# Optimization experiments

Measured on AMD Instinct MI355X. Metric: run time of the kernel, lower is better.

## Reference

```python
import jax, jax.numpy as jnp
import numpy as np

IDIM = 128   # idim == odim (fc1 input dim must match shift-slice width idim_q)
HDIM = 1024
CDIM = 256
IGNORE_OUT = 10000.0


def setup_inputs() -> dict:
    key = jax.random.key(0)
    ks = jax.random.split(key, 4)
    B, T = 4, 512
    x = jax.random.normal(ks[0], (B, T, IDIM), dtype=jnp.float32)
    y = jax.random.normal(ks[1], (B, T, IDIM), dtype=jnp.float32)
    # xavier-ish init for the two linears (bias zeroed, as in initialize())
    w1 = jax.random.normal(ks[2], (HDIM, IDIM), dtype=jnp.float32) / np.sqrt(IDIM).astype(np.float32)
    b1 = jnp.zeros((HDIM,), jnp.float32)
    w2 = jax.random.normal(ks[3], (IDIM, HDIM), dtype=jnp.float32) / np.sqrt(HDIM).astype(np.float32)
    b2 = jnpts = jnp.zeros((IDIM,), jnp.float32)
    return {"x": x, "y": y, "w1": w1, "b1": b1, "w2": w2, "b2": b2}


def _shift_stack(key_seq, idim):
    """Vectorized _pad_for_shift: (B,T,idim) -> (B,T,2*idim-1,idim) shifted slices."""
    pad = idim - 1
    kp = jnp.pad(key_seq, ((0, 0), (0, 0), (pad, pad)))  # (B,T,3*idim-2)
    idx = jnp.arange(2 * idim - 1)[:, None] + jnp.arange(idim)[None, :]  # (S, idim)
    return kp[..., idx]  # (B,T,S,idim)


def _forward(x, y, w1, b1, w2, b2):
    idim = IDIM
    n_iter = HDIM // CDIM
    seq_mask = (y == IGNORE_OUT)                      # (B,T,odim)
    denom = jnp.sum(~seq_mask).astype(x.dtype)
    y_res, x_res = y, x
    losses = []
    for i in range(n_iter):
        # --- argaug (scale=False): sliding cosine cross-correlation + argmax ---
        kpt = _shift_stack(x_res, idim)               # (B,T,S,idim), S=2*idim-1
        num = jnp.einsum('btd,btsd->bts', y_res, kpt)
        den = jnp.linalg.norm(y_res, axis=-1)[..., None] * jnp.linalg.norm(kpt, axis=-1)
        sim = jnp.where(den == 0, 0.0, num / jnp.where(den == 0, 1.0, den))  # NaN(0/0) -> 0
        idx = jnp.argmax(sim, axis=-1)                # (B,T), first max like torch.max
        x_aug = jnp.take_along_axis(kpt, idx[..., None, None], axis=2)[..., 0, :]  # (B,T,idim)
        # --- attention (detached) ---
        attn = jax.lax.stop_gradient(jax.nn.softmax(x_aug * y_res, axis=-1))
        x_attn = x_aug * attn
        # --- _reverse_pad_for_shift: un-shift x_attn by 2*idim-2 - idx ---
        pad = idim - 1
        xap = jnp.pad(x_attn, ((0, 0), (0, 0), (pad, pad)))
        ridx = (2 * idim - 2 - idx)[..., None] + jnp.arange(idim)  # (B,T,idim)
        x_ele = jnp.take_along_axis(xap, ridx, axis=-1)
        # --- channel-masked two-layer MLP ---
        h = x_attn @ w1.T + b1                        # (B,T,hdim)
        m = jnp.zeros((HDIM,), x.dtype).at[i * CDIM:(i + 1) * CDIM].set(1.0)
        y_ele = (h * m) @ w2.T + b2                   # (B,T,odim)
        # --- masked MSE (sum of masked squared errors / #unmasked) ---
        sq = jnp.where(seq_mask, 0.0, (y_ele - y_res) ** 2)
        losses.append(jnp.sum(sq) / denom)
        y_res = y_res - y_ele
        x_res = x_res - x_ele
    return jnp.mean(jnp.stack(losses))


def reference(x, y, w1, b1, w2, b2):
    return _forward(x, y, w1, b1, w2, b2)
```

## Files before the change

### kernel.cpp

```cpp
#include <hip/hip_runtime.h>
#include <math.h>

#define NROWS   2048
#define NITER   4
#define IGNORE_OUT 10000.0f

__global__ __launch_bounds__(128)
void prepK(const float* __restrict__ w1, const float* __restrict__ b1,
           const float* __restrict__ w2, const float* __restrict__ b2,
           float* __restrict__ Mt2, float* __restrict__ biasT, float* __restrict__ acc){
  const int blk = blockIdx.x;
  const int u = threadIdx.x;
  if (blk < 512){
    int i = blk >> 7, o = blk & 127;
    const float* w1p = w1 + (i * 256) * 128 + u;
    const float* w2p = w2 + o * 1024 + i * 256;
    float a = 0.f;
    #pragma unroll 16
    for (int c = 0; c < 256; ++c) a = fmaf(w1p[c * 128], w2p[c], a);
    Mt2[(i * 128 + o) * 128 + u] = a;
  } else if (blk < 516){
    int i = blk - 512;
    const float* w2p = w2 + u * 1024 + i * 256;
    const float* b1p = b1 + i * 256;
    float a = b2[u];
    #pragma unroll 8
    for (int c = 0; c < 256; ++c) a = fmaf(b1p[c], w2p[c], a);
    biasT[i * 128 + u] = a;
  } else {
    if (u < 2) acc[u] = 0.f;
  }
}

__global__ __launch_bounds__(64, 2)
void mainK(const float* __restrict__ x, const float* __restrict__ y,
           const float* __restrict__ Mt2, const float* __restrict__ biasT,
           float* __restrict__ acc){
  __shared__ alignas(16) float xr[128];
  __shared__ alignas(16) float xatt[128];
  __shared__ float yd[384];

  const int l = threadIdx.x;
  const long base = (long)blockIdx.x * 128;

  float xv0 = x[base + l],      xv1 = x[base + 64 + l];
  float yv0 = y[base + l],      yv1 = y[base + 64 + l];
  const bool m0 = (yv0 == IGNORE_OUT), m1 = (yv1 == IGNORE_OUT);
  float cnt = (m0 ? 0.f : 1.f) + (m1 ? 0.f : 1.f);
  float lossAcc = 0.f;

  xr[l] = xv0; xr[64 + l] = xv1;
  yd[128 + l] = yv0; yd[192 + l] = yv1;
  yd[256 + l] = yv0; yd[320 + l] = yv1;
  __syncthreads();

  for (int i = 0; i < NITER; ++i){
    float s0 = xv0 * xv0, s1 = xv1 * xv1;
    #pragma unroll
    for (int o2 = 1; o2 < 64; o2 <<= 1){
      float t0 = __shfl_up(s0, o2, 64);
      float t1 = __shfl_up(s1, o2, 64);
      if (l >= o2){ s0 += t0; s1 += t1; }
    }
    float tot0  = __shfl(s0, 63, 64);
    float prefA = s0;
    float prefB = s1 + tot0;
    float total = __shfl(s1, 63, 64) + tot0;

    float ny = yv0 * yv0 + yv1 * yv1;
    #pragma unroll
    for (int o2 = 32; o2; o2 >>= 1) ny += __shfl_xor(ny, o2, 64);
    float nY = sqrtf(ny);

    const float* ydpA = yd + (255 - l);
    const float* ydpB = yd + (191 - l);
    float ntA = 0.f, n1A = 0.f, ntB = 0.f, n1B = 0.f;
    #pragma unroll 4
    for (int j4 = 0; j4 < 64; j4 += 4){
      float4 x4 = *(const float4*)&xr[j4];
      float xx[4] = {x4.x, x4.y, x4.z, x4.w};
      #pragma unroll
      for (int e = 0; e < 4; ++e){
        int j = j4 + e;
        float pA = ydpA[j] * xx[e];
        float pB = ydpB[j] * xx[e];
        ntA += pA; n1A += (j <= l) ? pA : 0.f;
        ntB += pB; n1B += pB;
      }
    }
    #pragma unroll 4
    for (int j4 = 64; j4 < 128; j4 += 4){
      float4 x4 = *(const float4*)&xr[j4];
      float xx[4] = {x4.x, x4.y, x4.z, x4.w};
      #pragma unroll
      for (int e = 0; e < 4; ++e){
        int j = j4 + e;
        float pA = ydpA[j] * xx[e];
        float pB = ydpB[j] * xx[e];
        ntA += pA;
        ntB += pB; n1B += (j - 64 <= l) ? pB : 0.f;
      }
    }

    float bv; int bi;
    {
      float numA1 = n1A, numA2 = ntA - n1A;
      float numB1 = n1B, numB2 = ntB - n1B;
      float dA1 = nY * sqrtf(prefA);
      float dB1 = nY * sqrtf(prefB);
      float dA2 = nY * sqrtf(fmaxf(total - prefA, 0.f));
      float dB2 = nY * sqrtf(fmaxf(total - prefB, 0.f));
      float sA1 = (dA1 == 0.f) ? 0.f : numA1 / dA1;
      float sB1 = (dB1 == 0.f) ? 0.f : numB1 / dB1;
      float sA2 = (dA2 == 0.f) ? 0.f : numA2 / dA2;
      float sB2 = (dB2 == 0.f) ? 0.f : numB2 / dB2;
      if (l == 63) sB2 = -INFINITY;
      bv = sA1; bi = l;
      if (sB1 > bv){ bv = sB1; bi = l + 64;  }
      if (sA2 > bv){ bv = sA2; bi = l + 128; }
      if (sB2 > bv){ bv = sB2; bi = l + 192; }
    }
    #pragma unroll
    for (int o2 = 1; o2 < 64; o2 <<= 1){
      float ov = __shfl_xor(bv, o2, 64);
      int   oi = __shfl_xor(bi, o2, 64);
      if (ov > bv || (ov == bv && oi < bi)){ bv = ov; bi = oi; }
    }
    const int sstar = bi;

    int j0 = sstar + l - 127, j1 = j0 + 64;
    float xa0 = ((unsigned)j0 < 128u) ? xr[j0] : 0.f;
    float xa1 = ((unsigned)j1 < 128u) ? xr[j1] : 0.f;
    float z0 = xa0 * yv0, z1 = xa1 * yv1;
    float mz = fmaxf(z0, z1);
    #pragma unroll
    for (int o2 = 32; o2; o2 >>= 1) mz = fmaxf(mz, __shfl_xor(mz, o2, 64));
    float e0 = expf(z0 - mz), e1 = expf(z1 - mz);
    float se = e0 + e1;
    #pragma unroll
    for (int o2 = 32; o2; o2 >>= 1) se += __shfl_xor(se, o2, 64);
    float w0 = xa0 * (e0 / se), w1v = xa1 * (e1 / se);
    xatt[l] = w0; xatt[64 + l] = w1v;
    __syncthreads();

    int k0 = l + 127 - sstar, k1 = k0 + 64;
    xv0 -= ((unsigned)k0 < 128u) ? xatt[k0] : 0.f;
    xv1 -= ((unsigned)k1 < 128u) ? xatt[k1] : 0.f;
    xr[l] = xv0; xr[64 + l] = xv1;

    const float* MiA = Mt2 + (i * 128 + l) * 128;
    const float* MiB = MiA + 64 * 128;
    float aA = 0.f, aB = 0.f;
    #pragma unroll 4
    for (int d4 = 0; d4 < 128; d4 += 4){
      float4 xa4 = *(const float4*)&xatt[d4];
      float4 A4  = *(const float4*)&MiA[d4];
      float4 B4  = *(const float4*)&MiB[d4];
      aA = fmaf(A4.x, xa4.x, aA); aA = fmaf(A4.y, xa4.y, aA);
      aA = fmaf(A4.z, xa4.z, aA); aA = fmaf(A4.w, xa4.w, aA);
      aB = fmaf(B4.x, xa4.x, aB); aB = fmaf(B4.y, xa4.y, aB);
      aB = fmaf(B4.z, xa4.z, aB); aB = fmaf(B4.w, xa4.w, aB);
    }
    float ye0 = aA + biasT[i * 128 + l];
    float ye1 = aB + biasT[i * 128 + 64 + l];
    float d0 = ye0 - yv0, d1 = ye1 - yv1;
    if (!m0) lossAcc = fmaf(d0, d0, lossAcc);
    if (!m1) lossAcc = fmaf(d1, d1, lossAcc);
    yv0 = -d0; yv1 = -d1;
    yd[128 + l] = yv0; yd[192 + l] = yv1;
    yd[256 + l] = yv0; yd[320 + l] = yv1;
    __syncthreads();
  }

  #pragma unroll
  for (int o2 = 32; o2; o2 >>= 1){
    lossAcc += __shfl_xor(lossAcc, o2, 64);
    cnt     += __shfl_xor(cnt,     o2, 64);
  }
  if (l == 0){
    atomicAdd(&acc[0], lossAcc);
    atomicAdd(&acc[1], cnt);
  }
}

__global__ void finalize(const float* __restrict__ acc, float* __restrict__ out){
  if (threadIdx.x == 0 && blockIdx.x == 0)
    out[0] = acc[0] / ((float)NITER * acc[1]);
}

extern "C" void kernel_launch(void* const* d_in, const int* in_sizes, int n_in,
                              void* d_out, int out_size, void* d_ws, size_t ws_size,
                              hipStream_t stream){
  const float* x  = (const float*)d_in[0];
  const float* y  = (const float*)d_in[1];
  const float* w1 = (const float*)d_in[2];
  const float* b1 = (const float*)d_in[3];
  const float* w2 = (const float*)d_in[4];
  const float* b2 = (const float*)d_in[5];
  float* out = (float*)d_out;

  float* accp  = (float*)d_ws;
  float* Mt2   = (float*)((char*)d_ws + 256);
  float* biasT = (float*)((char*)d_ws + 256 + 4 * 128 * 128 * sizeof(float));

  prepK<<<517, 128, 0, stream>>>(w1, b1, w2, b2, Mt2, biasT, accp);
  mainK<<<NROWS, 64, 0, stream>>>(x, y, Mt2, biasT, accp);
  finalize<<<1, 64, 0, stream>>>(accp, out);
}
```

Baseline: 178.9 us.

## Process two rows per wave with register shuffles and fuse finalize via ticket

```diff
diff --git a/kernel.cpp b/kernel.cpp
--- a/kernel.cpp
+++ b/kernel.cpp
@@ -1,175 +1,246 @@
 #include <hip/hip_runtime.h>
 #include <math.h>
 
-#define NROWS   2048
-#define NITER   4
+#define NROWS 2048
+#define NBLK  1024
+#define NITER 4
 #define IGNORE_OUT 10000.0f
 
-__global__ __launch_bounds__(128)
+__device__ __forceinline__ float readlanef(float v, int lane){
+  return __int_as_float(__builtin_amdgcn_readlane(__float_as_int(v), lane));
+}
+__device__ __forceinline__ float rotup1(float v){
+  int i = __float_as_int(v);
+  return __int_as_float(__builtin_amdgcn_update_dpp(i, i, 0x13C, 0xF, 0xF, false));
+}
+__device__ __forceinline__ float gather128(float v0, float v1, int idx){
+  float g0 = __shfl(v0, idx & 63, 64);
+  float g1 = __shfl(v1, idx & 63, 64);
+  float r  = (idx & 64) ? g1 : g0;
+  return ((unsigned)idx < 128u) ? r : 0.f;
+}
+
+__global__ __launch_bounds__(256)
 void prepK(const float* __restrict__ w1, const float* __restrict__ b1,
            const float* __restrict__ w2, const float* __restrict__ b2,
-           float* __restrict__ Mt2, float* __restrict__ biasT, float* __restrict__ acc){
+           float* __restrict__ Mt2T, float* __restrict__ biasT, int* __restrict__ ticket){
+  __shared__ float part[256];
   const int blk = blockIdx.x;
   const int u = threadIdx.x;
   if (blk < 512){
     int i = blk >> 7, o = blk & 127;
-    const float* w1p = w1 + (i * 256) * 128 + u;
-    const float* w2p = w2 + o * 1024 + i * 256;
+    int d = u & 127, ch = u >> 7;
+    const float* w1p = w1 + (i * 256 + ch * 128) * 128 + d;
+    const float* w2p = w2 + o * 1024 + i * 256 + ch * 128;
     float a = 0.f;
     #pragma unroll 16
-    for (int c = 0; c < 256; ++c) a = fmaf(w1p[c * 128], w2p[c], a);
-    Mt2[(i * 128 + o) * 128 + u] = a;
+    for (int c = 0; c < 128; ++c) a = fmaf(w1p[c * 128], w2p[c], a);
+    part[u] = a;
+    __syncthreads();
+    if (u < 128) Mt2T[(i * 128 + u) * 128 + o] = part[u] + part[u + 128];
   } else if (blk < 516){
     int i = blk - 512;
-    const float* w2p = w2 + u * 1024 + i * 256;
-    const float* b1p = b1 + i * 256;
-    float a = b2[u];
-    #pragma unroll 8
-    for (int c = 0; c < 256; ++c) a = fmaf(b1p[c], w2p[c], a);
-    biasT[i * 128 + u] = a;
+    if (u < 128){
+      const float* w2p = w2 + u * 1024 + i * 256;
+      const float* b1p = b1 + i * 256;
+      float a = b2[u];
+      #pragma unroll 8
+      for (int c = 0; c < 256; ++c) a = fmaf(b1p[c], w2p[c], a);
+      biasT[i * 128 + u] = a;
+    }
   } else {
-    if (u < 2) acc[u] = 0.f;
-  }
-}
-
-__global__ __launch_bounds__(64, 2)
+    if (u == 0) *ticket = 0;
+  }
+}
+
+__global__ __launch_bounds__(64)
 void mainK(const float* __restrict__ x, const float* __restrict__ y,
-           const float* __restrict__ Mt2, const float* __restrict__ biasT,
-           float* __restrict__ acc){
-  __shared__ alignas(16) float xr[128];
-  __shared__ alignas(16) float xatt[128];
-  __shared__ float yd[384];
-
+           const float* __restrict__ Mt2T, const float* __restrict__ biasT,
+           unsigned long long* __restrict__ partials, int* __restrict__ ticket,
+           float* __restrict__ out){
   const int l = threadIdx.x;
-  const long base = (long)blockIdx.x * 128;
-
-  float xv0 = x[base + l],      xv1 = x[base + 64 + l];
-  float yv0 = y[base + l],      yv1 = y[base + 64 + l];
-  const bool m0 = (yv0 == IGNORE_OUT), m1 = (yv1 == IGNORE_OUT);
-  float cnt = (m0 ? 0.f : 1.f) + (m1 ? 0.f : 1.f);
+  const bool isl0 = (l == 0);
+  const long b0 = (long)blockIdx.x * 256;
+
+  float x0lo = x[b0 + l],        x0hi = x[b0 + 64 + l];
+  float x1lo = x[b0 + 128 + l],  x1hi = x[b0 + 192 + l];
+  float y0lo = y[b0 + l],        y0hi = y[b0 + 64 + l];
+  float y1lo = y[b0 + 128 + l],  y1hi = y[b0 + 192 + l];
+  const bool m0lo = (y0lo == IGNORE_OUT), m0hi = (y0hi == IGNORE_OUT);
+  const bool m1lo = (y1lo == IGNORE_OUT), m1hi = (y1hi == IGNORE_OUT);
+  float cnt = (m0lo?0.f:1.f) + (m0hi?0.f:1.f) + (m1lo?0.f:1.f) + (m1hi?0.f:1.f);
   float lossAcc = 0.f;
 
-  xr[l] = xv0; xr[64 + l] = xv1;
-  yd[128 + l] = yv0; yd[192 + l] = yv1;
-  yd[256 + l] = yv0; yd[320 + l] = yv1;
-  __syncthreads();
-
   for (int i = 0; i < NITER; ++i){
-    float s0 = xv0 * xv0, s1 = xv1 * xv1;
+    float p0a = x0lo * x0lo, p0b = x0hi * x0hi;
+    float p1a = x1lo * x1lo, p1b = x1hi * x1hi;
     #pragma unroll
     for (int o2 = 1; o2 < 64; o2 <<= 1){
-      float t0 = __shfl_up(s0, o2, 64);
-      float t1 = __shfl_up(s1, o2, 64);
-      if (l >= o2){ s0 += t0; s1 += t1; }
-    }
-    float tot0  = __shfl(s0, 63, 64);
-    float prefA = s0;
-    float prefB = s1 + tot0;
-    float total = __shfl(s1, 63, 64) + tot0;
-
-    float ny = yv0 * yv0 + yv1 * yv1;
+      float t0a = __shfl_up(p0a, o2, 64), t0b = __shfl_up(p0b, o2, 64);
+      float t1a = __shfl_up(p1a, o2, 64), t1b = __shfl_up(p1b, o2, 64);
+      if (l >= o2){ p0a += t0a; p0b += t0b; p1a += t1a; p1b += t1b; }
+    }
+    float tot0_0 = readlanef(p0a, 63), tot0_1 = readlanef(p1a, 63);
+    float prefA0 = p0a, prefB0 = p0b + tot0_0;
+    float prefA1 = p1a, prefB1 = p1b + tot0_1;
+    float total0 = readlanef(p0b, 63) + tot0_0;
+    float total1 = readlanef(p1b, 63) + tot0_1;
+
+    float ny0 = y0lo * y0lo + y0hi * y0hi;
+    float ny1 = y1lo * y1lo + y1hi * y1hi;
     #pragma unroll
-    for (int o2 = 32; o2; o2 >>= 1) ny += __shfl_xor(ny, o2, 64);
-    float nY = sqrtf(ny);
-
-    const float* ydpA = yd + (255 - l);
-    const float* ydpB = yd + (191 - l);
-    float ntA = 0.f, n1A = 0.f, ntB = 0.f, n1B = 0.f;
-    #pragma unroll 4
-    for (int j4 = 0; j4 < 64; j4 += 4){
-      float4 x4 = *(const float4*)&xr[j4];
-      float xx[4] = {x4.x, x4.y, x4.z, x4.w};
-      #pragma unroll
-      for (int e = 0; e < 4; ++e){
-        int j = j4 + e;
-        float pA = ydpA[j] * xx[e];
-        float pB = ydpB[j] * xx[e];
-        ntA += pA; n1A += (j <= l) ? pA : 0.f;
-        ntB += pB; n1B += pB;
-      }
-    }
-    #pragma unroll 4
-    for (int j4 = 64; j4 < 128; j4 += 4){
-      float4 x4 = *(const float4*)&xr[j4];
-      float xx[4] = {x4.x, x4.y, x4.z, x4.w};
-      #pragma unroll
-      for (int e = 0; e < 4; ++e){
-        int j = j4 + e;
-        float pA = ydpA[j] * xx[e];
-        float pB = ydpB[j] * xx[e];
-        ntA += pA;
-        ntB += pB; n1B += (j - 64 <= l) ? pB : 0.f;
-      }
-    }
-
-    float bv; int bi;
-    {
-      float numA1 = n1A, numA2 = ntA - n1A;
-      float numB1 = n1B, numB2 = ntB - n1B;
-      float dA1 = nY * sqrtf(prefA);
-      float dB1 = nY * sqrtf(prefB);
-      float dA2 = nY * sqrtf(fmaxf(total - prefA, 0.f));
-      float dB2 = nY * sqrtf(fmaxf(total - prefB, 0.f));
-      float sA1 = (dA1 == 0.f) ? 0.f : numA1 / dA1;
-      float sB1 = (dB1 == 0.f) ? 0.f : numB1 / dB1;
-      float sA2 = (dA2 == 0.f) ? 0.f : numA2 / dA2;
-      float sB2 = (dB2 == 0.f) ? 0.f : numB2 / dB2;
+    for (int o2 = 32; o2; o2 >>= 1){
+      ny0 += __shfl_xor(ny0, o2, 64);
+      ny1 += __shfl_xor(ny1, o2, 64);
+    }
+
+    float a0 = __shfl(y0hi, 63 - l, 64), b0r = __shfl(y0lo, 63 - l, 64);
+    float a1 = __shfl(y1hi, 63 - l, 64), b1r = __shfl(y1lo, 63 - l, 64);
+    float ntA0 = 0.f, n1A0 = 0.f, ntB0 = 0.f, n1B0 = 0.f;
+    float ntA1 = 0.f, n1A1 = 0.f, ntB1 = 0.f, n1B1 = 0.f;
+    #pragma unroll 4
+    for (int j = 0; j < 64; ++j){
+      float sx0 = readlanef(x0lo, j);
+      float sx1 = readlanef(x1lo, j);
+      ntA0 = fmaf(a0, sx0, ntA0);  ntB0 = fmaf(b0r, sx0, ntB0);
+      ntA1 = fmaf(a1, sx1, ntA1);  ntB1 = fmaf(b1r, sx1, ntB1);
+      bool snap = (j == l);
+      n1A0 = snap ? ntA0 : n1A0;
+      n1A1 = snap ? ntA1 : n1A1;
+      float r0 = rotup1(a0), r1 = rotup1(b0r);
+      a0  = isl0 ? r1 : r0;  b0r = isl0 ? r0 : r1;
+      float r2 = rotup1(a1), r3 = rotup1(b1r);
+      a1  = isl0 ? r3 : r2;  b1r = isl0 ? r2 : r3;
+    }
+    #pragma unroll 4
+    for (int j = 64; j < 128; ++j){
+      float sx0 = readlanef(x0hi, j - 64);
+      float sx1 = readlanef(x1hi, j - 64);
+      ntA0 = fmaf(a0, sx0, ntA0);  ntB0 = fmaf(b0r, sx0, ntB0);
+      ntA1 = fmaf(a1, sx1, ntA1);  ntB1 = fmaf(b1r, sx1, ntB1);
+      bool snap = ((j - 64) == l);
+      n1B0 = snap ? ntB0 : n1B0;
+      n1B1 = snap ? ntB1 : n1B1;
+      float r0 = rotup1(a0), r1 = rotup1(b0r);
+      a0  = isl0 ? r1 : r0;  b0r = isl0 ? r0 : r1;
+      float r2 = rotup1(a1), r3 = rotup1(b1r);
+      a1  = isl0 ? r3 : r2;  b1r = isl0 ? r2 : r3;
+    }
+
+    int sstar0, sstar1;
+    {
+      float nY = sqrtf(ny0);
+      float dA1 = nY * sqrtf(prefA0),                    dB1 = nY * sqrtf(prefB0);
+      float dA2 = nY * sqrtf(fmaxf(total0 - prefA0, 0.f)), dB2 = nY * sqrtf(fmaxf(total0 - prefB0, 0.f));
+      float sA1 = (dA1 == 0.f) ? 0.f : n1A0 / dA1;
+      float sB1 = (dB1 == 0.f) ? 0.f : n1B0 / dB1;
+      float sA2 = (dA2 == 0.f) ? 0.f : (ntA0 - n1A0) / dA2;
+      float sB2 = (dB2 == 0.f) ? 0.f : (ntB0 - n1B0) / dB2;
       if (l == 63) sB2 = -INFINITY;
-      bv = sA1; bi = l;
+      float bv = sA1; int bi = l;
       if (sB1 > bv){ bv = sB1; bi = l + 64;  }
       if (sA2 > bv){ bv = sA2; bi = l + 128; }
       if (sB2 > bv){ bv = sB2; bi = l + 192; }
-    }
-    #pragma unroll
-    for (int o2 = 1; o2 < 64; o2 <<= 1){
-      float ov = __shfl_xor(bv, o2, 64);
-      int   oi = __shfl_xor(bi, o2, 64);
-      if (ov > bv || (ov == bv && oi < bi)){ bv = ov; bi = oi; }
-    }
-    const int sstar = bi;
-
-    int j0 = sstar + l - 127, j1 = j0 + 64;
-    float xa0 = ((unsigned)j0 < 128u) ? xr[j0] : 0.f;
-    float xa1 = ((unsigned)j1 < 128u) ? xr[j1] : 0.f;
-    float z0 = xa0 * yv0, z1 = xa1 * yv1;
-    float mz = fmaxf(z0, z1);
-    #pragma unroll
-    for (int o2 = 32; o2; o2 >>= 1) mz = fmaxf(mz, __shfl_xor(mz, o2, 64));
-    float e0 = expf(z0 - mz), e1 = expf(z1 - mz);
-    float se = e0 + e1;
-    #pragma unroll
-    for (int o2 = 32; o2; o2 >>= 1) se += __shfl_xor(se, o2, 64);
-    float w0 = xa0 * (e0 / se), w1v = xa1 * (e1 / se);
-    xatt[l] = w0; xatt[64 + l] = w1v;
-    __syncthreads();
-
-    int k0 = l + 127 - sstar, k1 = k0 + 64;
-    xv0 -= ((unsigned)k0 < 128u) ? xatt[k0] : 0.f;
-    xv1 -= ((unsigned)k1 < 128u) ? xatt[k1] : 0.f;
-    xr[l] = xv0; xr[64 + l] = xv1;
-
-    const float* MiA = Mt2 + (i * 128 + l) * 128;
-    const float* MiB = MiA + 64 * 128;
-    float aA = 0.f, aB = 0.f;
-    #pragma unroll 4
-    for (int d4 = 0; d4 < 128; d4 += 4){
-      float4 xa4 = *(const float4*)&xatt[d4];
-      float4 A4  = *(const float4*)&MiA[d4];
-      float4 B4  = *(const float4*)&MiB[d4];
-      aA = fmaf(A4.x, xa4.x, aA); aA = fmaf(A4.y, xa4.y, aA);
-      aA = fmaf(A4.z, xa4.z, aA); aA = fmaf(A4.w, xa4.w, aA);
-      aB = fmaf(B4.x, xa4.x, aB); aB = fmaf(B4.y, xa4.y, aB);
-      aB = fmaf(B4.z, xa4.z, aB); aB = fmaf(B4.w, xa4.w, aB);
-    }
-    float ye0 = aA + biasT[i * 128 + l];
-    float ye1 = aB + biasT[i * 128 + 64 + l];
-    float d0 = ye0 - yv0, d1 = ye1 - yv1;
-    if (!m0) lossAcc = fmaf(d0, d0, lossAcc);
-    if (!m1) lossAcc = fmaf(d1, d1, lossAcc);
-    yv0 = -d0; yv1 = -d1;
-    yd[128 + l] = yv0; yd[192 + l] = yv1;
-    yd[256 + l] = yv0; yd[320 + l] = yv1;
-    __syncthreads();
+      #pragma unroll
+      for (int o2 = 1; o2 < 64; o2 <<= 1){
+        float ov = __shfl_xor(bv, o2, 64);
+        int   oi = __shfl_xor(bi, o2, 64);
+        if (ov > bv || (ov == bv && oi < bi)){ bv = ov; bi = oi; }
+      }
+      sstar0 = bi;
+    }
+    {
+      float nY = sqrtf(ny1);
+      float dA1 = nY * sqrtf(prefA1),                    dB1 = nY * sqrtf(prefB1);
+      float dA2 = nY * sqrtf(fmaxf(total1 - prefA1, 0.f)), dB2 = nY * sqrtf(fmaxf(total1 - prefB1, 0.f));
+      float sA1 = (dA1 == 0.f) ? 0.f : n1A1 / dA1;
+      float sB1 = (dB1 == 0.f) ? 0.f : n1B1 / dB1;
+      float sA2 = (dA2 == 0.f) ? 0.f : (ntA1 - n1A1) / dA2;
+      float sB2 = (dB2 == 0.f) ? 0.f : (ntB1 - n1B1) / dB2;
+      if (l == 63) sB2 = -INFINITY;
+      float bv = sA1; int bi = l;
+      if (sB1 > bv){ bv = sB1; bi = l + 64;  }
+      if (sA2 > bv){ bv = sA2; bi = l + 128; }
+      if (sB2 > bv){ bv = sB2; bi = l + 192; }
+      #pragma unroll
+      for (int o2 = 1; o2 < 64; o2 <<= 1){
+        float ov = __shfl_xor(bv, o2, 64);
+        int   oi = __shfl_xor(bi, o2, 64);
+        if (ov > bv || (ov == bv && oi < bi)){ bv = ov; bi = oi; }
+      }
+      sstar1 = bi;
+    }
+
+    float w0lo, w0hi, w1lo, w1hi;
+    {
+      int j0 = sstar0 + l - 127;
+      float xa = gather128(x0lo, x0hi, j0);
+      float xb = gather128(x0lo, x0hi, j0 + 64);
+      float za = xa * y0lo, zb = xb * y0hi;
+      float mz = fmaxf(za, zb);
+      #pragma unroll
+      for (int o2 = 32; o2; o2 >>= 1) mz = fmaxf(mz, __shfl_xor(mz, o2, 64));
+      float ea = expf(za - mz), eb = expf(zb - mz);
+      float se = ea + eb;
+      #pragma unroll
+      for (int o2 = 32; o2; o2 >>= 1) se += __shfl_xor(se, o2, 64);
+      w0lo = xa * (ea / se); w0hi = xb * (eb / se);
+      int k0 = l + 127 - sstar0;
+      x0lo -= gather128(w0lo, w0hi, k0);
+      x0hi -= gather128(w0lo, w0hi, k0 + 64);
+    }
+    {
+      int j0 = sstar1 + l - 127;
+      float xa = gather128(x1lo, x1hi, j0);
+      float xb = gather128(x1lo, x1hi, j0 + 64);
+      float za = xa * y1lo, zb = xb * y1hi;
+      float mz = fmaxf(za, zb);
+      #pragma unroll
+      for (int o2 = 32; o2; o2 >>= 1) mz = fmaxf(mz, __shfl_xor(mz, o2, 64));
+      float ea = expf(za - mz), eb = expf(zb - mz);
+      float se = ea + eb;
+      #pragma unroll
+      for (int o2 = 32; o2; o2 >>= 1) se += __shfl_xor(se, o2, 64);
+      w1lo = xa * (ea / se); w1hi = xb * (eb / se);
+      int k0 = l + 127 - sstar1;
+      x1lo -= gather128(w1lo, w1hi, k0);
+      x1hi -= gather128(w1lo, w1hi, k0 + 64);
+    }
+
+    const float* Mi = Mt2T + i * 16384;
+    float aA0 = 0.f, aB0 = 0.f, aA1 = 0.f, aB1 = 0.f;
+    #pragma unroll 4
+    for (int d = 0; d < 64; ++d){
+      float mlo = Mi[d * 128 + l];
+      float mhi = Mi[d * 128 + 64 + l];
+      float s0 = readlanef(w0lo, d);
+      float s1 = readlanef(w1lo, d);
+      aA0 = fmaf(mlo, s0, aA0); aB0 = fmaf(mhi, s0, aB0);
+      aA1 = fmaf(mlo, s1, aA1); aB1 = fmaf(mhi, s1, aB1);
+    }
+    #pragma unroll 4
+    for (int d = 64; d < 128; ++d){
+      float mlo = Mi[d * 128 + l];
+      float mhi = Mi[d * 128 + 64 + l];
+      float s0 = readlanef(w0hi, d - 64);
+      float s1 = readlanef(w1hi, d - 64);
+      aA0 = fmaf(mlo, s0, aA0); aB0 = fmaf(mhi, s0, aB0);
+      aA1 = fmaf(mlo, s1, aA1); aB1 = fmaf(mhi, s1, aB1);
+    }
+    float blo = biasT[i * 128 + l], bhi = biasT[i * 128 + 64 + l];
+
+    {
+      float dlo = (aA0 + blo) - y0lo, dhi = (aB0 + bhi) - y0hi;
+      if (!m0lo) lossAcc = fmaf(dlo, dlo, lossAcc);
+      if (!m0hi) lossAcc = fmaf(dhi, dhi, lossAcc);
+      y0lo = -dlo; y0hi = -dhi;
+    }
+    {
+      float dlo = (aA1 + blo) - y1lo, dhi = (aB1 + bhi) - y1hi;
+      if (!m1lo) lossAcc = fmaf(dlo, dlo, lossAcc);
+      if (!m1hi) lossAcc = fmaf(dhi, dhi, lossAcc);
+      y1lo = -dlo; y1hi = -dhi;
+    }
   }
 
   #pragma unroll
@@ -177,15 +248,28 @@
     lossAcc += __shfl_xor(lossAcc, o2, 64);
     cnt     += __shfl_xor(cnt,     o2, 64);
   }
+  int old = 0;
   if (l == 0){
-    atomicAdd(&acc[0], lossAcc);
-    atomicAdd(&acc[1], cnt);
-  }
-}
-
-__global__ void finalize(const float* __restrict__ acc, float* __restrict__ out){
-  if (threadIdx.x == 0 && blockIdx.x == 0)
-    out[0] = acc[0] / ((float)NITER * acc[1]);
+    union { float2 f; unsigned long long u; } pk;
+    pk.f.x = lossAcc; pk.f.y = cnt;
+    __hip_atomic_store(&partials[blockIdx.x], pk.u, __ATOMIC_RELEASE, __HIP_MEMORY_SCOPE_AGENT);
+    old = __hip_atomic_fetch_add(ticket, 1, __ATOMIC_ACQ_REL, __HIP_MEMORY_SCOPE_AGENT);
+  }
+  old = __shfl(old, 0, 64);
+  if (old == NBLK - 1){
+    float ls = 0.f, cs = 0.f;
+    for (int g = l; g < NBLK; g += 64){
+      union { float2 f; unsigned long long u; } pk;
+      pk.u = __hip_atomic_load(&partials[g], __ATOMIC_ACQUIRE, __HIP_MEMORY_SCOPE_AGENT);
+      ls += pk.f.x; cs += pk.f.y;
+    }
+    #pragma unroll
+    for (int o2 = 32; o2; o2 >>= 1){
+      ls += __shfl_xor(ls, o2, 64);
+      cs += __shfl_xor(cs, o2, 64);
+    }
+    if (l == 0) out[0] = ls / ((float)NITER * cs);
+  }
 }
 
 extern "C" void kernel_launch(void* const* d_in, const int* in_sizes, int n_in,
@@ -199,11 +283,12 @@
   const float* b2 = (const float*)d_in[5];
   float* out = (float*)d_out;
 
-  float* accp  = (float*)d_ws;
-  float* Mt2   = (float*)((char*)d_ws + 256);
-  float* biasT = (float*)((char*)d_ws + 256 + 4 * 128 * 128 * sizeof(float));
-
-  prepK<<<517, 128, 0, stream>>>(w1, b1, w2, b2, Mt2, biasT, accp);
-  mainK<<<NROWS, 64, 0, stream>>>(x, y, Mt2, biasT, accp);
-  finalize<<<1, 64, 0, stream>>>(accp, out);
-}
+  int*   ticket = (int*)d_ws;
+  float* Mt2T   = (float*)((char*)d_ws + 256);
+  float* biasT  = (float*)((char*)d_ws + 256 + 4 * 128 * 128 * sizeof(float));
+  unsigned long long* partials =
+      (unsigned long long*)((char*)d_ws + 256 + 4 * 128 * 128 * sizeof(float) + 4 * 128 * sizeof(float));
+
+  prepK<<<517, 256, 0, stream>>>(w1, b1, w2, b2, Mt2T, biasT, ticket);
+  mainK<<<NBLK, 64, 0, stream>>>(x, y, Mt2T, biasT, partials, ticket, out);
+}
```

Measured after the change: 182.6 us. 2.1% more time.

## Rewrite main kernel with two waves per row, register-only cross-correlation and fused finalize

Applied to the files above, without the earlier changes.

```diff
diff --git a/kernel.cpp b/kernel.cpp
--- a/kernel.cpp
+++ b/kernel.cpp
@@ -1,14 +1,39 @@
 #include <hip/hip_runtime.h>
 #include <math.h>
 
-#define NROWS   2048
-#define NITER   4
+#define NROWS 2048
+#define NBLK  2048
+#define NITER 4
 #define IGNORE_OUT 10000.0f
+
+__device__ __forceinline__ float readlanef(float v, int lane){
+  return __int_as_float(__builtin_amdgcn_readlane(__float_as_int(v), lane));
+}
+__device__ __forceinline__ float rotup1(float v){
+  int i = __float_as_int(v);
+  return __int_as_float(__builtin_amdgcn_update_dpp(i, i, 0x13C, 0xF, 0xF, false));
+}
+__device__ __forceinline__ float gather128(float v0, float v1, int idx){
+  float g0 = __shfl(v0, idx & 63, 64);
+  float g1 = __shfl(v1, idx & 63, 64);
+  float r  = (idx & 64) ? g1 : g0;
+  return ((unsigned)idx < 128u) ? r : 0.f;
+}
+__device__ __forceinline__ float bflySum(float v){
+  #pragma unroll
+  for (int o = 32; o; o >>= 1) v += __shfl_xor(v, o, 64);
+  return v;
+}
+__device__ __forceinline__ float bflyMax(float v){
+  #pragma unroll
+  for (int o = 32; o; o >>= 1) v = fmaxf(v, __shfl_xor(v, o, 64));
+  return v;
+}
 
 __global__ __launch_bounds__(128)
 void prepK(const float* __restrict__ w1, const float* __restrict__ b1,
            const float* __restrict__ w2, const float* __restrict__ b2,
-           float* __restrict__ Mt2, float* __restrict__ biasT, float* __restrict__ acc){
+           float* __restrict__ M4, float* __restrict__ biasT, int* __restrict__ ticket){
   const int blk = blockIdx.x;
   const int u = threadIdx.x;
   if (blk < 512){
@@ -18,7 +43,7 @@
     float a = 0.f;
     #pragma unroll 16
     for (int c = 0; c < 256; ++c) a = fmaf(w1p[c * 128], w2p[c], a);
-    Mt2[(i * 128 + o) * 128 + u] = a;
+    M4[i * 16384 + (u >> 2) * 512 + o * 4 + (u & 3)] = a;
   } else if (blk < 516){
     int i = blk - 512;
     const float* w2p = w2 + u * 1024 + i * 256;
@@ -28,164 +53,189 @@
     for (int c = 0; c < 256; ++c) a = fmaf(b1p[c], w2p[c], a);
     biasT[i * 128 + u] = a;
   } else {
-    if (u < 2) acc[u] = 0.f;
-  }
-}
-
-__global__ __launch_bounds__(64, 2)
+    if (u == 0) *ticket = 0;
+  }
+}
+
+__global__ __launch_bounds__(128, 4)
 void mainK(const float* __restrict__ x, const float* __restrict__ y,
-           const float* __restrict__ Mt2, const float* __restrict__ biasT,
-           float* __restrict__ acc){
-  __shared__ alignas(16) float xr[128];
-  __shared__ alignas(16) float xatt[128];
-  __shared__ float yd[384];
-
-  const int l = threadIdx.x;
+           const float* __restrict__ M4, const float* __restrict__ biasT,
+           unsigned long long* __restrict__ partials, int* __restrict__ ticket,
+           float* __restrict__ out){
+  __shared__ float sVal[2];
+  __shared__ int   sIdx[2];
+  __shared__ float yel[128];
+  __shared__ float sL[2], sC[2];
+  __shared__ int   sOld;
+
+  const int u = threadIdx.x;
+  const int l = u & 63;
+  const int w = u >> 6;
+  const bool isl0 = (l == 0);
   const long base = (long)blockIdx.x * 128;
 
-  float xv0 = x[base + l],      xv1 = x[base + 64 + l];
-  float yv0 = y[base + l],      yv1 = y[base + 64 + l];
-  const bool m0 = (yv0 == IGNORE_OUT), m1 = (yv1 == IGNORE_OUT);
-  float cnt = (m0 ? 0.f : 1.f) + (m1 ? 0.f : 1.f);
+  float xlo = x[base + l],      xhi = x[base + 64 + l];
+  float ylo = y[base + l],      yhi = y[base + 64 + l];
+  const bool mlo = (ylo == IGNORE_OUT), mhi = (yhi == IGNORE_OUT);
+  const bool ownM = w ? mhi : mlo;
+  float cnt = ownM ? 0.f : 1.f;
   float lossAcc = 0.f;
 
-  xr[l] = xv0; xr[64 + l] = xv1;
-  yd[128 + l] = yv0; yd[192 + l] = yv1;
-  yd[256 + l] = yv0; yd[320 + l] = yv1;
-  __syncthreads();
-
   for (int i = 0; i < NITER; ++i){
-    float s0 = xv0 * xv0, s1 = xv1 * xv1;
+    float sq_lo = xlo * xlo, sq_hi = xhi * xhi;
+    float v = w ? sq_hi : sq_lo;
     #pragma unroll
     for (int o2 = 1; o2 < 64; o2 <<= 1){
-      float t0 = __shfl_up(s0, o2, 64);
-      float t1 = __shfl_up(s1, o2, 64);
-      if (l >= o2){ s0 += t0; s1 += t1; }
-    }
-    float tot0  = __shfl(s0, 63, 64);
-    float prefA = s0;
-    float prefB = s1 + tot0;
-    float total = __shfl(s1, 63, 64) + tot0;
-
-    float ny = yv0 * yv0 + yv1 * yv1;
-    #pragma unroll
-    for (int o2 = 32; o2; o2 >>= 1) ny += __shfl_xor(ny, o2, 64);
-    float nY = sqrtf(ny);
-
-    const float* ydpA = yd + (255 - l);
-    const float* ydpB = yd + (191 - l);
-    float ntA = 0.f, n1A = 0.f, ntB = 0.f, n1B = 0.f;
-    #pragma unroll 4
-    for (int j4 = 0; j4 < 64; j4 += 4){
-      float4 x4 = *(const float4*)&xr[j4];
-      float xx[4] = {x4.x, x4.y, x4.z, x4.w};
+      float tv = __shfl_up(v, o2, 64);
+      if (l >= o2) v += tv;
+    }
+    float osum  = bflySum(w ? sq_lo : sq_hi);
+    float total = readlanef(v, 63) + osum;
+    float pref_t = w ? (v + osum) : v;
+
+    float nY = sqrtf(bflySum(ylo * ylo + yhi * yhi));
+
+    float nt = 0.f, n1 = 0.f;
+    {
+      float src0 = w ? ylo : yhi;
+      float win = __shfl(src0, 63 - l, 64);
+      if (w == 0){
+        #pragma unroll 8
+        for (int j = 0; j < 64; ++j){
+          float sx = readlanef(xlo, j);
+          nt = fmaf(win, sx, nt);
+          n1 = (j == l) ? nt : n1;
+          float inc = readlanef(ylo, j);
+          float r = rotup1(win);
+          win = isl0 ? inc : r;
+        }
+        #pragma unroll 8
+        for (int j = 0; j < 64; ++j){
+          float sx = readlanef(xhi, j);
+          nt = fmaf(win, sx, nt);
+          float inc = readlanef(yhi, j);
+          float r = rotup1(win);
+          win = isl0 ? inc : r;
+        }
+      } else {
+        #pragma unroll 8
+        for (int j = 0; j < 64; ++j){
+          float sx = readlanef(xlo, j);
+          nt = fmaf(win, sx, nt);
+          float inc = readlanef(yhi, j);
+          float r = rotup1(win);
+          win = isl0 ? inc : r;
+        }
+        #pragma unroll 8
+        for (int j = 0; j < 64; ++j){
+          float sx = readlanef(xhi, j);
+          nt = fmaf(win, sx, nt);
+          n1 = (j == l) ? nt : n1;
+          float inc = readlanef(ylo, j);
+          float r = rotup1(win);
+          win = isl0 ? inc : r;
+        }
+      }
+    }
+
+    {
+      float num1 = n1, num2 = nt - n1;
+      float d1 = nY * sqrtf(pref_t);
+      float d2 = nY * sqrtf(fmaxf(total - pref_t, 0.f));
+      float s1 = (d1 == 0.f) ? 0.f : num1 / d1;
+      float s2 = (d2 == 0.f) ? 0.f : num2 / d2;
+      int tsh = (w << 6) | l;
+      if (tsh == 127) s2 = -INFINITY;
+      float bv = s1; int bi = tsh;
+      if (s2 > bv){ bv = s2; bi = tsh + 128; }
       #pragma unroll
-      for (int e = 0; e < 4; ++e){
-        int j = j4 + e;
-        float pA = ydpA[j] * xx[e];
-        float pB = ydpB[j] * xx[e];
-        ntA += pA; n1A += (j <= l) ? pA : 0.f;
-        ntB += pB; n1B += pB;
-      }
-    }
-    #pragma unroll 4
-    for (int j4 = 64; j4 < 128; j4 += 4){
-      float4 x4 = *(const float4*)&xr[j4];
-      float xx[4] = {x4.x, x4.y, x4.z, x4.w};
+      for (int o2 = 1; o2 < 64; o2 <<= 1){
+        float ov = __shfl_xor(bv, o2, 64);
+        int   oi = __shfl_xor(bi, o2, 64);
+        if (ov > bv || (ov == bv && oi < bi)){ bv = ov; bi = oi; }
+      }
+      if (l == 0){ sVal[w] = bv; sIdx[w] = bi; }
+    }
+    __syncthreads();
+    int sstar;
+    {
+      float v0 = sVal[0], v1 = sVal[1];
+      int   i0 = sIdx[0], i1 = sIdx[1];
+      sstar = (v1 > v0 || (v1 == v0 && i1 < i0)) ? i1 : i0;
+    }
+
+    int j0 = sstar + l - 127;
+    float xa = gather128(xlo, xhi, j0);
+    float xb = gather128(xlo, xhi, j0 + 64);
+    float za = xa * ylo, zb = xb * yhi;
+    float mz = bflyMax(fmaxf(za, zb));
+    float ea = expf(za - mz), eb = expf(zb - mz);
+    float se = bflySum(ea + eb);
+    float wlo = xa * (ea / se), whi = xb * (eb / se);
+
+    int k0 = l + 127 - sstar;
+    xlo -= gather128(wlo, whi, k0);
+    xhi -= gather128(wlo, whi, k0 + 64);
+
+    float ye;
+    {
+      const float4* Mp = (const float4*)(M4 + (size_t)i * 16384);
+      float av = 0.f;
       #pragma unroll
-      for (int e = 0; e < 4; ++e){
-        int j = j4 + e;
-        float pA = ydpA[j] * xx[e];
-        float pB = ydpB[j] * xx[e];
-        ntA += pA;
-        ntB += pB; n1B += (j - 64 <= l) ? pB : 0.f;
-      }
-    }
-
-    float bv; int bi;
-    {
-      float numA1 = n1A, numA2 = ntA - n1A;
-      float numB1 = n1B, numB2 = ntB - n1B;
-      float dA1 = nY * sqrtf(prefA);
-      float dB1 = nY * sqrtf(prefB);
-      float dA2 = nY * sqrtf(fmaxf(total - prefA, 0.f));
-      float dB2 = nY * sqrtf(fmaxf(total - prefB, 0.f));
-      float sA1 = (dA1 == 0.f) ? 0.f : numA1 / dA1;
-      float sB1 = (dB1 == 0.f) ? 0.f : numB1 / dB1;
-      float sA2 = (dA2 == 0.f) ? 0.f : numA2 / dA2;
-      float sB2 = (dB2 == 0.f) ? 0.f : numB2 / dB2;
-      if (l == 63) sB2 = -INFINITY;
-      bv = sA1; bi = l;
-      if (sB1 > bv){ bv = sB1; bi = l + 64;  }
-      if (sA2 > bv){ bv = sA2; bi = l + 128; }
-      if (sB2 > bv){ bv = sB2; bi = l + 192; }
-    }
-    #pragma unroll
-    for (int o2 = 1; o2 < 64; o2 <<= 1){
-      float ov = __shfl_xor(bv, o2, 64);
-      int   oi = __shfl_xor(bi, o2, 64);
-      if (ov > bv || (ov == bv && oi < bi)){ bv = ov; bi = oi; }
-    }
-    const int sstar = bi;
-
-    int j0 = sstar + l - 127, j1 = j0 + 64;
-    float xa0 = ((unsigned)j0 < 128u) ? xr[j0] : 0.f;
-    float xa1 = ((unsigned)j1 < 128u) ? xr[j1] : 0.f;
-    float z0 = xa0 * yv0, z1 = xa1 * yv1;
-    float mz = fmaxf(z0, z1);
-    #pragma unroll
-    for (int o2 = 32; o2; o2 >>= 1) mz = fmaxf(mz, __shfl_xor(mz, o2, 64));
-    float e0 = expf(z0 - mz), e1 = expf(z1 - mz);
-    float se = e0 + e1;
-    #pragma unroll
-    for (int o2 = 32; o2; o2 >>= 1) se += __shfl_xor(se, o2, 64);
-    float w0 = xa0 * (e0 / se), w1v = xa1 * (e1 / se);
-    xatt[l] = w0; xatt[64 + l] = w1v;
+      for (int dd = 0; dd < 16; ++dd){
+        float4 m = Mp[dd * 128 + u];
+        av = fmaf(m.x, readlanef(wlo, 4 * dd + 0), av);
+        av = fmaf(m.y, readlanef(wlo, 4 * dd + 1), av);
+        av = fmaf(m.z, readlanef(wlo, 4 * dd + 2), av);
+        av = fmaf(m.w, readlanef(wlo, 4 * dd + 3), av);
+      }
+      #pragma unroll
+      for (int dd = 16; dd < 32; ++dd){
+        float4 m = Mp[dd * 128 + u];
+        int b = 4 * dd - 64;
+        av = fmaf(m.x, readlanef(whi, b + 0), av);
+        av = fmaf(m.y, readlanef(whi, b + 1), av);
+        av = fmaf(m.z, readlanef(whi, b + 2), av);
+        av = fmaf(m.w, readlanef(whi, b + 3), av);
+      }
+      ye = av + biasT[i * 128 + u];
+    }
+    {
+      float yown = w ? yhi : ylo;
+      float dOwn = ye - yown;
+      if (!ownM) lossAcc = fmaf(dOwn, dOwn, lossAcc);
+    }
+    yel[u] = ye;
     __syncthreads();
-
-    int k0 = l + 127 - sstar, k1 = k0 + 64;
-    xv0 -= ((unsigned)k0 < 128u) ? xatt[k0] : 0.f;
-    xv1 -= ((unsigned)k1 < 128u) ? xatt[k1] : 0.f;
-    xr[l] = xv0; xr[64 + l] = xv1;
-
-    const float* MiA = Mt2 + (i * 128 + l) * 128;
-    const float* MiB = MiA + 64 * 128;
-    float aA = 0.f, aB = 0.f;
-    #pragma unroll 4
-    for (int d4 = 0; d4 < 128; d4 += 4){
-      float4 xa4 = *(const float4*)&xatt[d4];
-      float4 A4  = *(const float4*)&MiA[d4];
-      float4 B4  = *(const float4*)&MiB[d4];
-      aA = fmaf(A4.x, xa4.x, aA); aA = fmaf(A4.y, xa4.y, aA);
-      aA = fmaf(A4.z, xa4.z, aA); aA = fmaf(A4.w, xa4.w, aA);
-      aB = fmaf(B4.x, xa4.x, aB); aB = fmaf(B4.y, xa4.y, aB);
-      aB = fmaf(B4.z, xa4.z, aB); aB = fmaf(B4.w, xa4.w, aB);
-    }
-    float ye0 = aA + biasT[i * 128 + l];
-    float ye1 = aB + biasT[i * 128 + 64 + l];
-    float d0 = ye0 - yv0, d1 = ye1 - yv1;
-    if (!m0) lossAcc = fmaf(d0, d0, lossAcc);
-    if (!m1) lossAcc = fmaf(d1, d1, lossAcc);
-    yv0 = -d0; yv1 = -d1;
-    yd[128 + l] = yv0; yd[192 + l] = yv1;
-    yd[256 + l] = yv0; yd[320 + l] = yv1;
+    {
+      float dlo = yel[l] - ylo, dhi = yel[64 + l] - yhi;
+      ylo = -dlo; yhi = -dhi;
+    }
+  }
+
+  lossAcc = bflySum(lossAcc);
+  cnt     = bflySum(cnt);
+  if (l == 0){ sL[w] = lossAcc; sC[w] = cnt; }
+  __syncthreads();
+  if (u == 0){
+    union { float2 f; unsigned long long v; } pk;
+    pk.f.x = sL[0] + sL[1]; pk.f.y = sC[0] + sC[1];
+    __hip_atomic_store(&partials[blockIdx.x], pk.v, __ATOMIC_RELEASE, __HIP_MEMORY_SCOPE_AGENT);
+    sOld = __hip_atomic_fetch_add(ticket, 1, __ATOMIC_ACQ_REL, __HIP_MEMORY_SCOPE_AGENT);
+  }
+  __syncthreads();
+  if (sOld == NBLK - 1){
+    float ls = 0.f, cs = 0.f;
+    for (int g = u; g < NBLK; g += 128){
+      union { float2 f; unsigned long long v; } pk;
+      pk.v = __hip_atomic_load(&partials[g], __ATOMIC_ACQUIRE, __HIP_MEMORY_SCOPE_AGENT);
+      ls += pk.f.x; cs += pk.f.y;
+    }
+    ls = bflySum(ls); cs = bflySum(cs);
+    if (l == 0){ sL[w] = ls; sC[w] = cs; }
     __syncthreads();
-  }
-
-  #pragma unroll
-  for (int o2 = 32; o2; o2 >>= 1){
-    lossAcc += __shfl_xor(lossAcc, o2, 64);
-    cnt     += __shfl_xor(cnt,     o2, 64);
-  }
-  if (l == 0){
-    atomicAdd(&acc[0], lossAcc);
-    atomicAdd(&acc[1], cnt);
-  }
-}
-
-__global__ void finalize(const float* __restrict__ acc, float* __restrict__ out){
-  if (threadIdx.x == 0 && blockIdx.x == 0)
-    out[0] = acc[0] / ((float)NITER * acc[1]);
+    if (u == 0) out[0] = (sL[0] + sL[1]) / ((float)NITER * (sC[0] + sC[1]));
+  }
 }
 
 extern "C" void kernel_launch(void* const* d_in, const int* in_sizes, int n_in,
@@ -199,11 +249,12 @@
   const float* b2 = (const float*)d_in[5];
   float* out = (float*)d_out;
 
-  float* accp  = (float*)d_ws;
-  float* Mt2   = (float*)((char*)d_ws + 256);
-  float* biasT = (float*)((char*)d_ws + 256 + 4 * 128 * 128 * sizeof(float));
-
-  prepK<<<517, 128, 0, stream>>>(w1, b1, w2, b2, Mt2, biasT, accp);
-  mainK<<<NROWS, 64, 0, stream>>>(x, y, Mt2, biasT, accp);
-  finalize<<<1, 64, 0, stream>>>(accp, out);
-}
+  int*   ticket = (int*)d_ws;
+  float* M4     = (float*)((char*)d_ws + 256);
+  float* biasT  = (float*)((char*)d_ws + 256 + 4 * 128 * 128 * sizeof(float));
+  unsigned long long* partials =
+      (unsigned long long*)((char*)d_ws + 256 + 4 * 128 * 128 * sizeof(float) + 4 * 128 * sizeof(float));
+
+  prepK<<<517, 128, 0, stream>>>(w1, b1, w2, b2, M4, biasT, ticket);
+  mainK<<<NBLK, 128, 0, stream>>>(x, y, M4, biasT, partials, ticket, out);
+}
```

After: 166.1 us. -7.1%, faster.
